# Kernel tuning notes

Measured on AMD Instinct MI355X. Metric: run time of the kernel, lower is better.

The kernel has to match this reference:

```python
import jax, jax.numpy as jnp
import numpy as np

B, T, C = 2, 4096, 512
H, DH = 8, 64            # num_heads, num_head_channels (per-head dim after reshape)
COND = 512
SCALE = (DH // H) ** -0.5  # faithful to original: (num_head_channels // num_heads)**-0.5


def setup_inputs() -> dict:
    key = jax.random.key(0)
    ks = jax.random.split(key, 6)
    x = jax.random.normal(ks[0], (B, T, C), dtype=jnp.float32)
    condition = jax.random.normal(ks[1], (B, T, COND), dtype=jnp.float32)
    W_qk = jax.random.normal(ks[2], (COND, 2 * H * DH), dtype=jnp.float32) * (COND ** -0.5)
    W_v = jax.random.normal(ks[3], (C, H * DH), dtype=jnp.float32) * (C ** -0.5)
    W_u = jax.random.normal(ks[4], (H * DH, C), dtype=jnp.float32) * ((H * DH) ** -0.5)
    b_u = jax.random.normal(ks[5], (C,), dtype=jnp.float32) * 0.01
    return {"x": x, "condition": condition, "W_qk": W_qk, "W_v": W_v, "W_u": W_u, "b_u": b_u}


def reference(x, condition, W_qk, W_v, W_u, b_u):
    b, t, _ = x.shape
    qk = condition @ W_qk                                  # [b, t, 2*H*DH]
    q, k = jnp.split(qk, 2, axis=-1)
    q = q.reshape(b, t, H, DH).transpose(0, 2, 1, 3)       # [b, H, t, DH]
    k = k.reshape(b, t, H, DH).transpose(0, 2, 1, 3)
    v = (x @ W_v).reshape(b, t, H, DH).transpose(0, 2, 1, 3)
    q = q * SCALE
    dots = jnp.einsum('bhid,bhjd->bhij', q, k)             # [b, H, t, t] (1 GB score matrix)
    attn = jax.nn.softmax(dots, axis=-1)
    out = jnp.einsum('bhij,bhjd->bhid', attn, v)           # [b, H, t, DH]
    out = out.transpose(0, 2, 1, 3).reshape(b, t, H * DH)
    return out @ W_u + b_u
```

## Files before the change

kernel.cpp:

```cpp
#include <hip/hip_runtime.h>

#define B_SZ 2
#define T_SZ 4096

typedef unsigned short u16;
typedef __attribute__((ext_vector_type(8))) short short8;
typedef __attribute__((ext_vector_type(4))) float f32x4;
typedef __attribute__((ext_vector_type(4))) unsigned short u16x4;

#define CEXP 0.51006973f

__device__ __forceinline__ u16 f2bf(float f) {
    unsigned int u;
    __builtin_memcpy(&u, &f, 4);
    u = (u + 0x7fffu + ((u >> 16) & 1u)) >> 16;
    return (u16)u;
}
__device__ __forceinline__ unsigned int rbits(float f) {
    unsigned int u;
    __builtin_memcpy(&u, &f, 4);
    return u + 0x8000u;
}
__device__ __forceinline__ f32x4 mfma16(short8 a, short8 b, f32x4 c) {
    return __builtin_amdgcn_mfma_f32_16x16x32_bf16(a, b, c, 0, 0, 0);
}

__global__ void k_prep(const float* __restrict__ Wqk, const float* __restrict__ Wv,
                       const float* __restrict__ Wu, u16* __restrict__ Wqk_t,
                       u16* __restrict__ Wv_t, u16* __restrict__ Wu_t) {
    int blk = blockIdx.x;
    if (blk < 2048) {
        int idx = blk * 256 + threadIdx.x;
        Wqk_t[(size_t)(idx & 1023) * 512 + (idx >> 10)] = f2bf(Wqk[idx]);
    } else if (blk < 3072) {
        int idx = (blk - 2048) * 256 + threadIdx.x;
        Wv_t[(size_t)(idx & 511) * 512 + (idx >> 9)] = f2bf(Wv[idx]);
    } else {
        int idx = (blk - 3072) * 256 + threadIdx.x;
        Wu_t[(size_t)(idx & 511) * 512 + (idx >> 9)] = f2bf(Wu[idx]);
    }
}

template <typename OutT, int MODE, bool AF32, bool BF32, int TM, int TN>
__global__ __launch_bounds__(256) void k_gemm4(const void* __restrict__ Ap, const void* __restrict__ Bp,
                                               const float* __restrict__ bias, OutT* __restrict__ C,
                                               OutT* __restrict__ C2) {
    const int K = 512;
    constexpr int MI = TM / 32, NJ = TN / 32;
    constexpr int NAF = TM / 32, NAB = TM / 64;
    constexpr int NBF = TN / 32, NBB = TN / 64;
    int m0 = blockIdx.x * TM, n0 = blockIdx.y * TN;
    int tid = threadIdx.x;
    int wave = tid >> 6, lane = tid & 63, l16 = lane & 15, q = lane >> 4;
    int mo = (wave & 1) * (TM / 2), no = (wave >> 1) * (TN / 2);

    __shared__ __align__(16) u16 As[TM * 72];
    __shared__ __align__(16) u16 Bs[TN * 72];

    f32x4 acc[MI][NJ];
#pragma unroll
    for (int i = 0; i < MI; ++i)
#pragma unroll
        for (int j = 0; j < NJ; ++j) acc[i][j] = (f32x4){0.f, 0.f, 0.f, 0.f};

    const float* Af = (const float*)Ap; const u16* Ab = (const u16*)Ap;
    const float* Bf = (const float*)Bp; const u16* Bb = (const u16*)Bp;

    const float* apf[NAF > 0 ? NAF : 1]; const u16* apb[NAB > 0 ? NAB : 1];
    const float* bpf[NBF > 0 ? NBF : 1]; const u16* bpb[NBB > 0 ? NBB : 1];
    float4 raf[NAF > 0 ? NAF : 1], rbf[NBF > 0 ? NBF : 1];
    short8 rab[NAB > 0 ? NAB : 1], rbb[NBB > 0 ? NBB : 1];

    if constexpr (AF32) {
#pragma unroll
        for (int jj = 0; jj < NAF; ++jj) {
            int id = tid + 256 * jj;
            apf[jj] = Af + (size_t)(m0 + (id >> 3)) * K + (id & 7) * 4;
            raf[jj] = *(const float4*)(apf[jj]);
        }
    } else {
#pragma unroll
        for (int jj = 0; jj < NAB; ++jj) {
            int id = tid + 256 * jj;
            apb[jj] = Ab + (size_t)(m0 + (id >> 2)) * K + (id & 3) * 8;
            rab[jj] = *(const short8*)(apb[jj]);
        }
    }
    if constexpr (BF32) {
#pragma unroll
        for (int jj = 0; jj < NBF; ++jj) {
            int id = tid + 256 * jj;
            bpf[jj] = Bf + (size_t)(n0 + (id >> 3)) * K + (id & 7) * 4;
            rbf[jj] = *(const float4*)(bpf[jj]);
        }
    } else {
#pragma unroll
        for (int jj = 0; jj < NBB; ++jj) {
            int id = tid + 256 * jj;
            bpb[jj] = Bb + (size_t)(n0 + (id >> 2)) * K + (id & 3) * 8;
            rbb[jj] = *(const short8*)(bpb[jj]);
        }
    }

#pragma unroll 1
    for (int k0 = 0; k0 < K; k0 += 32) {
        __syncthreads();
        if constexpr (AF32) {
#pragma unroll
            for (int jj = 0; jj < NAF; ++jj) {
                int id = tid + 256 * jj;
                u16x4 w = { f2bf(raf[jj].x), f2bf(raf[jj].y), f2bf(raf[jj].z), f2bf(raf[jj].w) };
                *(u16x4*)(&As[(id >> 3) * 72 + (id & 7) * 4]) = w;
            }
        } else {
#pragma unroll
            for (int jj = 0; jj < NAB; ++jj) {
                int id = tid + 256 * jj;
                *(short8*)(&As[(id >> 2) * 72 + (id & 3) * 8]) = rab[jj];
            }
        }
        if constexpr (BF32) {
#pragma unroll
            for (int jj = 0; jj < NBF; ++jj) {
                int id = tid + 256 * jj;
                u16x4 w = { f2bf(rbf[jj].x), f2bf(rbf[jj].y), f2bf(rbf[jj].z), f2bf(rbf[jj].w) };
                *(u16x4*)(&Bs[(id >> 3) * 72 + (id & 7) * 4]) = w;
            }
        } else {
#pragma unroll
            for (int jj = 0; jj < NBB; ++jj) {
                int id = tid + 256 * jj;
                *(short8*)(&Bs[(id >> 2) * 72 + (id & 3) * 8]) = rbb[jj];
            }
        }
        __syncthreads();

        int kadv = (k0 + 32 < K) ? 32 : 0;
        if constexpr (AF32) {
#pragma unroll
            for (int jj = 0; jj < NAF; ++jj) { apf[jj] += kadv; raf[jj] = *(const float4*)(apf[jj]); }
        } else {
#pragma unroll
            for (int jj = 0; jj < NAB; ++jj) { apb[jj] += kadv; rab[jj] = *(const short8*)(apb[jj]); }
        }
        if constexpr (BF32) {
#pragma unroll
            for (int jj = 0; jj < NBF; ++jj) { bpf[jj] += kadv; rbf[jj] = *(const float4*)(bpf[jj]); }
        } else {
#pragma unroll
            for (int jj = 0; jj < NBB; ++jj) { bpb[jj] += kadv; rbb[jj] = *(const short8*)(bpb[jj]); }
        }
        __builtin_amdgcn_sched_barrier(0);

        short8 af[MI], bf[NJ];
#pragma unroll
        for (int i = 0; i < MI; ++i) af[i] = *(const short8*)(&As[(mo + i * 16 + l16) * 72 + q * 8]);
#pragma unroll
        for (int j = 0; j < NJ; ++j) bf[j] = *(const short8*)(&Bs[(no + j * 16 + l16) * 72 + q * 8]);
#pragma unroll
        for (int i = 0; i < MI; ++i)
#pragma unroll
            for (int j = 0; j < NJ; ++j) acc[i][j] = mfma16(af[i], bf[j], acc[i][j]);
    }

#pragma unroll
    for (int i = 0; i < MI; ++i) {
        int mb = m0 + mo + i * 16 + q * 4;
#pragma unroll
        for (int j = 0; j < NJ; ++j) {
            int nc = n0 + no + j * 16 + l16;
            if constexpr (MODE == 0) {
                float4 bb = *(const float4*)(bias + mb);
                float4 w = { acc[i][j][0] + bb.x, acc[i][j][1] + bb.y,
                             acc[i][j][2] + bb.z, acc[i][j][3] + bb.w };
                *(float4*)(&C[(size_t)nc * 512 + mb]) = w;
            } else if constexpr (MODE == 1) {
                int b = nc >> 12, t = nc & 4095;
                int h = (mb & 511) >> 6, d = mb & 63;
                size_t addr = ((size_t)((b * 8 + h) * 4096 + t)) * 64 + d;
                if (mb < 512) {
                    u16x4 w = { f2bf(acc[i][j][0] * CEXP), f2bf(acc[i][j][1] * CEXP),
                                f2bf(acc[i][j][2] * CEXP), f2bf(acc[i][j][3] * CEXP) };
                    *(u16x4*)(&C[addr]) = w;
                } else {
                    u16x4 w = { f2bf(acc[i][j][0]), f2bf(acc[i][j][1]),
                                f2bf(acc[i][j][2]), f2bf(acc[i][j][3]) };
                    *(u16x4*)(&C2[addr]) = w;
                }
            } else {
                int b = mb >> 12, t = mb & 4095;
                int kt = t >> 6, k64 = t & 63;
                int h = nc >> 6, d = nc & 63;
                size_t addr = ((((size_t)(b * 8 + h) * 64 + kt) * 64 + d) << 6) + k64;
                u16x4 w = { f2bf(acc[i][j][0]), f2bf(acc[i][j][1]),
                            f2bf(acc[i][j][2]), f2bf(acc[i][j][3]) };
                *(u16x4*)(&C[addr]) = w;
            }
        }
    }
}

__global__ __launch_bounds__(256) void k_flash(const u16* __restrict__ Qh, const u16* __restrict__ Kh,
                                               const u16* __restrict__ Vb, u16* __restrict__ o) {
    int bid = blockIdx.x;
    int h = bid & 7, qt = (bid >> 3) & 31, b = bid >> 8;
    int tid = threadIdx.x;
    int wave = tid >> 6, lane = tid & 63, l16 = lane & 15, q = lane >> 4;

    __shared__ __align__(16) u16 Kt[64 * 80];
    __shared__ __align__(16) u16 Vt[64 * 72];

    int head = b * 8 + h;
    short8 qf[2][2];
#pragma unroll
    for (int g = 0; g < 2; ++g) {
        const u16* qp = Qh + ((size_t)head * 4096 + qt * 128 + g * 64 + wave * 16 + l16) * 64 + q * 8;
        qf[g][0] = *(const short8*)(qp);
        qf[g][1] = *(const short8*)(qp + 32);
    }

    const u16* kb = Kh + (size_t)head * 4096 * 64;
    const u16* vb = Vb + (size_t)head * 4096 * 64;

    int r0 = tid >> 3, g0 = tid & 7;
    u16* kw0 = &Kt[r0 * 80 + g0 * 8];
    u16* kw1 = &Kt[(r0 + 32) * 80 + g0 * 8];
    u16* vw0 = &Vt[r0 * 72 + g0 * 8];
    u16* vw1 = &Vt[(r0 + 32) * 72 + g0 * 8];

    f32x4 oacc[2][4];
#pragma unroll
    for (int g = 0; g < 2; ++g)
#pragma unroll
        for (int c = 0; c < 4; ++c) oacc[g][c] = (f32x4){0.f, 0.f, 0.f, 0.f};
    f32x4 lacc[2];
    lacc[0] = (f32x4){0.f, 0.f, 0.f, 0.f};
    lacc[1] = (f32x4){0.f, 0.f, 0.f, 0.f};
    const short8 ones = { 0x3F80, 0x3F80, 0x3F80, 0x3F80, 0x3F80, 0x3F80, 0x3F80, 0x3F80 };
    int pi0 = (l16 >> 2) * 8 + (l16 & 3);

    int start = qt * 2;
    size_t off0 = (size_t)((start) & 63) * 4096;
    short8 rk0 = *(const short8*)(kb + off0 + tid * 8);
    short8 rk1 = *(const short8*)(kb + off0 + tid * 8 + 2048);
    short8 rv0 = *(const short8*)(vb + off0 + tid * 8);
    short8 rv1 = *(const short8*)(vb + off0 + tid * 8 + 2048);

#pragma unroll 1
    for (int it = 0; it < 64; ++it) {
        __syncthreads();
        *(short8*)kw0 = rk0;
        *(short8*)kw1 = rk1;
        *(short8*)vw0 = rv0;
        *(short8*)vw1 = rv1;
        __syncthreads();

        size_t offn = (size_t)((start + it + 1) & 63) * 4096;
        rk0 = *(const short8*)(kb + offn + tid * 8);
        rk1 = *(const short8*)(kb + offn + tid * 8 + 2048);
        rv0 = *(const short8*)(vb + offn + tid * 8);
        rv1 = *(const short8*)(vb + offn + tid * 8 + 2048);
        __builtin_amdgcn_sched_barrier(0);

#pragma unroll
        for (int kk = 0; kk < 2; ++kk) {
            const u16* ka = &Kt[(kk * 32 + pi0) * 80 + q * 8];
            short8 A00 = *(const short8*)(ka);
            short8 A01 = *(const short8*)(ka + 32);
            short8 A10 = *(const short8*)(ka + 4 * 80);
            short8 A11 = *(const short8*)(ka + 4 * 80 + 32);
            short8 vfc[4];
#pragma unroll
            for (int c = 0; c < 4; ++c)
                vfc[c] = *(const short8*)(&Vt[(c * 16 + l16) * 72 + kk * 32 + q * 8]);

#pragma unroll
            for (int g = 0; g < 2; ++g) {
                f32x4 s0 = (f32x4){0.f, 0.f, 0.f, 0.f};
                f32x4 s1 = (f32x4){0.f, 0.f, 0.f, 0.f};
                s0 = mfma16(A00, qf[g][0], s0); s0 = mfma16(A01, qf[g][1], s0);
                s1 = mfma16(A10, qf[g][0], s1); s1 = mfma16(A11, qf[g][1], s1);

                uint4 pd;
                pd.x = __builtin_amdgcn_perm(rbits(__builtin_amdgcn_exp2f(s0[1])),
                                             rbits(__builtin_amdgcn_exp2f(s0[0])), 0x07060302u);
                pd.y = __builtin_amdgcn_perm(rbits(__builtin_amdgcn_exp2f(s0[3])),
                                             rbits(__builtin_amdgcn_exp2f(s0[2])), 0x07060302u);
                pd.z = __builtin_amdgcn_perm(rbits(__builtin_amdgcn_exp2f(s1[1])),
                                             rbits(__builtin_amdgcn_exp2f(s1[0])), 0x07060302u);
                pd.w = __builtin_amdgcn_perm(rbits(__builtin_amdgcn_exp2f(s1[3])),
                                             rbits(__builtin_amdgcn_exp2f(s1[2])), 0x07060302u);
                short8 pf;
                __builtin_memcpy(&pf, &pd, 16);

                lacc[g] = mfma16(ones, pf, lacc[g]);
#pragma unroll
                for (int c = 0; c < 4; ++c)
                    oacc[g][c] = mfma16(vfc[c], pf, oacc[g][c]);
            }
        }
    }

#pragma unroll
    for (int g = 0; g < 2; ++g) {
        float inv = 1.f / lacc[g][0];
        u16* ob = o + (size_t)(b * T_SZ + qt * 128 + g * 64 + wave * 16 + l16) * 512 + h * 64 + q * 4;
#pragma unroll
        for (int c = 0; c < 4; ++c) {
            u16x4 w = { f2bf(oacc[g][c][0] * inv), f2bf(oacc[g][c][1] * inv),
                        f2bf(oacc[g][c][2] * inv), f2bf(oacc[g][c][3] * inv) };
            *(u16x4*)(ob + c * 16) = w;
        }
    }
}

extern "C" void kernel_launch(void* const* d_in, const int* in_sizes, int n_in,
                              void* d_out, int out_size, void* d_ws, size_t ws_size,
                              hipStream_t stream) {
    const float* x    = (const float*)d_in[0];
    const float* cond = (const float*)d_in[1];
    const float* Wqk  = (const float*)d_in[2];
    const float* Wv   = (const float*)d_in[3];
    const float* Wu   = (const float*)d_in[4];
    const float* bu   = (const float*)d_in[5];
    float* out = (float*)d_out;

    const size_t MT = (size_t)B_SZ * T_SZ;
    u16* qh_ws = (u16*)d_ws;
    u16* kh_ws = qh_ws + MT * 512;
    u16* vb_ws = kh_ws + MT * 512;
    u16* at_ws = vb_ws + MT * 512;
    u16* Wqk_t = at_ws + MT * 512;
    u16* Wv_t  = Wqk_t + (size_t)1024 * 512;
    u16* Wu_t  = Wv_t + (size_t)512 * 512;

    k_prep<<<4096, 256, 0, stream>>>(Wqk, Wv, Wu, Wqk_t, Wv_t, Wu_t);

    k_gemm4<u16, 1, false, true, 256, 64><<<dim3(4, 128), 256, 0, stream>>>(Wqk_t, cond, nullptr, qh_ws, kh_ws);
    k_gemm4<u16, 2, true, false, 64, 128><<<dim3(128, 4), 256, 0, stream>>>(x, Wv_t, nullptr, vb_ws, nullptr);
    k_flash<<<512, 256, 0, stream>>>(qh_ws, kh_ws, vb_ws, at_ws);
    k_gemm4<float, 0, false, false, 128, 64><<<dim3(4, 128), 256, 0, stream>>>(Wu_t, at_ws, bu, out, nullptr);
}
```

Baseline: 235.2 us.

## Split flash KV range across two wave groups, merge QKV GEMMs, tile weight prep

```diff
diff --git a/kernel.cpp b/kernel.cpp
--- a/kernel.cpp
+++ b/kernel.cpp
@@ -28,34 +28,43 @@
 __global__ void k_prep(const float* __restrict__ Wqk, const float* __restrict__ Wv,
                        const float* __restrict__ Wu, u16* __restrict__ Wqk_t,
                        u16* __restrict__ Wv_t, u16* __restrict__ Wu_t) {
-    int blk = blockIdx.x;
-    if (blk < 2048) {
-        int idx = blk * 256 + threadIdx.x;
-        Wqk_t[(size_t)(idx & 1023) * 512 + (idx >> 10)] = f2bf(Wqk[idx]);
-    } else if (blk < 3072) {
-        int idx = (blk - 2048) * 256 + threadIdx.x;
-        Wv_t[(size_t)(idx & 511) * 512 + (idx >> 9)] = f2bf(Wv[idx]);
-    } else {
-        int idx = (blk - 3072) * 256 + threadIdx.x;
-        Wu_t[(size_t)(idx & 511) * 512 + (idx >> 9)] = f2bf(Wu[idx]);
+    int blk = blockIdx.x, tid = threadIdx.x;
+    __shared__ u16 T[64][72];
+    const float* src; u16* dst; int N, ti;
+    if (blk < 128)      { src = Wqk; dst = Wqk_t; N = 1024; ti = blk; }
+    else if (blk < 192) { src = Wv;  dst = Wv_t;  N = 512;  ti = blk - 128; }
+    else                { src = Wu;  dst = Wu_t;  N = 512;  ti = blk - 192; }
+    int nt = N >> 6;
+    int bi = ti / nt, bj = ti - bi * nt;
+    int kb = bi * 64, nb = bj * 64;
+    int r = tid >> 2, c4 = (tid & 3) * 16;
+#pragma unroll
+    for (int jj = 0; jj < 4; ++jj) {
+        float4 v = *(const float4*)(src + (size_t)(kb + r) * N + nb + c4 + jj * 4);
+        u16x4 w = { f2bf(v.x), f2bf(v.y), f2bf(v.z), f2bf(v.w) };
+        *(u16x4*)(&T[r][c4 + jj * 4]) = w;
+    }
+    __syncthreads();
+#pragma unroll
+    for (int jj = 0; jj < 4; ++jj) {
+        int c = c4 + jj * 4;
+        u16x4 w = { T[c][r], T[c + 1][r], T[c + 2][r], T[c + 3][r] };
+        *(u16x4*)(dst + (size_t)(nb + r) * 512 + kb + c) = w;
     }
 }
 
 template <typename OutT, int MODE, bool AF32, bool BF32, int TM, int TN>
-__global__ __launch_bounds__(256) void k_gemm4(const void* __restrict__ Ap, const void* __restrict__ Bp,
-                                               const float* __restrict__ bias, OutT* __restrict__ C,
-                                               OutT* __restrict__ C2) {
+__device__ __forceinline__ void gemm_body(int m0, int n0,
+                                          const void* __restrict__ Ap, const void* __restrict__ Bp,
+                                          const float* __restrict__ bias, OutT* __restrict__ C,
+                                          OutT* __restrict__ C2, u16* As, u16* Bs) {
     const int K = 512;
     constexpr int MI = TM / 32, NJ = TN / 32;
     constexpr int NAF = TM / 32, NAB = TM / 64;
     constexpr int NBF = TN / 32, NBB = TN / 64;
-    int m0 = blockIdx.x * TM, n0 = blockIdx.y * TN;
     int tid = threadIdx.x;
     int wave = tid >> 6, lane = tid & 63, l16 = lane & 15, q = lane >> 4;
     int mo = (wave & 1) * (TM / 2), no = (wave >> 1) * (TN / 2);
-
-    __shared__ __align__(16) u16 As[TM * 72];
-    __shared__ __align__(16) u16 Bs[TN * 72];
 
     f32x4 acc[MI][NJ];
 #pragma unroll
@@ -200,21 +209,51 @@
     }
 }
 
-__global__ __launch_bounds__(256) void k_flash(const u16* __restrict__ Qh, const u16* __restrict__ Kh,
+__global__ __launch_bounds__(256) void k_qkv(const u16* __restrict__ Wqk_t, const float* __restrict__ cond,
+                                             const float* __restrict__ x, const u16* __restrict__ Wv_t,
+                                             u16* __restrict__ Qh, u16* __restrict__ Kh,
+                                             u16* __restrict__ Vb) {
+    __shared__ __align__(16) u16 smem[(128 + 64) * 72];
+    u16* As = smem;
+    u16* Bs = smem + 128 * 72;
+    int bid = blockIdx.x;
+    if (bid < 1024) {
+        int bx = bid >> 7, by = bid & 127;
+        gemm_body<u16, 1, false, true, 128, 64>(bx * 128, by * 64, Wqk_t, cond, nullptr, Qh, Kh, As, Bs);
+    } else {
+        int bid2 = bid - 1024;
+        int by = bid2 >> 6, bx = bid2 & 63;
+        gemm_body<u16, 2, true, false, 128, 64>(bx * 128, by * 64, x, Wv_t, nullptr, Vb, nullptr, As, Bs);
+    }
+}
+
+__global__ __launch_bounds__(256) void k_out(const u16* __restrict__ Wu_t, const u16* __restrict__ at,
+                                             const float* __restrict__ bu, float* __restrict__ out) {
+    __shared__ __align__(16) u16 smem[(64 + 64) * 72];
+    int bid = blockIdx.x;
+    int bx = bid >> 7, by = bid & 127;
+    gemm_body<float, 0, false, false, 64, 64>(bx * 64, by * 64, Wu_t, at, bu, out, nullptr,
+                                              smem, smem + 64 * 72);
+}
+
+__global__ __launch_bounds__(512) void k_flash(const u16* __restrict__ Qh, const u16* __restrict__ Kh,
                                                const u16* __restrict__ Vb, u16* __restrict__ o) {
     int bid = blockIdx.x;
     int h = bid & 7, qt = (bid >> 3) & 31, b = bid >> 8;
     int tid = threadIdx.x;
     int wave = tid >> 6, lane = tid & 63, l16 = lane & 15, q = lane >> 4;
-
-    __shared__ __align__(16) u16 Kt[64 * 80];
-    __shared__ __align__(16) u16 Vt[64 * 72];
+    int ks = wave >> 2, w4 = wave & 3;
+    int t256 = tid & 255;
+
+    __shared__ __align__(16) u16 smem[2 * (64 * 80 + 64 * 72)];
+    u16* Kt = smem + ks * (64 * 80 + 64 * 72);
+    u16* Vt = Kt + 64 * 80;
 
     int head = b * 8 + h;
     short8 qf[2][2];
 #pragma unroll
     for (int g = 0; g < 2; ++g) {
-        const u16* qp = Qh + ((size_t)head * 4096 + qt * 128 + g * 64 + wave * 16 + l16) * 64 + q * 8;
+        const u16* qp = Qh + ((size_t)head * 4096 + qt * 128 + g * 64 + w4 * 16 + l16) * 64 + q * 8;
         qf[g][0] = *(const short8*)(qp);
         qf[g][1] = *(const short8*)(qp + 32);
     }
@@ -222,7 +261,7 @@
     const u16* kb = Kh + (size_t)head * 4096 * 64;
     const u16* vb = Vb + (size_t)head * 4096 * 64;
 
-    int r0 = tid >> 3, g0 = tid & 7;
+    int r0 = t256 >> 3, g0 = t256 & 7;
     u16* kw0 = &Kt[r0 * 80 + g0 * 8];
     u16* kw1 = &Kt[(r0 + 32) * 80 + g0 * 8];
     u16* vw0 = &Vt[r0 * 72 + g0 * 8];
@@ -239,15 +278,14 @@
     const short8 ones = { 0x3F80, 0x3F80, 0x3F80, 0x3F80, 0x3F80, 0x3F80, 0x3F80, 0x3F80 };
     int pi0 = (l16 >> 2) * 8 + (l16 & 3);
 
-    int start = qt * 2;
-    size_t off0 = (size_t)((start) & 63) * 4096;
-    short8 rk0 = *(const short8*)(kb + off0 + tid * 8);
-    short8 rk1 = *(const short8*)(kb + off0 + tid * 8 + 2048);
-    short8 rv0 = *(const short8*)(vb + off0 + tid * 8);
-    short8 rv1 = *(const short8*)(vb + off0 + tid * 8 + 2048);
+    size_t off0 = (size_t)(ks * 32 + (qt & 31)) * 4096;
+    short8 rk0 = *(const short8*)(kb + off0 + t256 * 8);
+    short8 rk1 = *(const short8*)(kb + off0 + t256 * 8 + 2048);
+    short8 rv0 = *(const short8*)(vb + off0 + t256 * 8);
+    short8 rv1 = *(const short8*)(vb + off0 + t256 * 8 + 2048);
 
 #pragma unroll 1
-    for (int it = 0; it < 64; ++it) {
+    for (int it = 0; it < 32; ++it) {
         __syncthreads();
         *(short8*)kw0 = rk0;
         *(short8*)kw1 = rk1;
@@ -255,11 +293,11 @@
         *(short8*)vw1 = rv1;
         __syncthreads();
 
-        size_t offn = (size_t)((start + it + 1) & 63) * 4096;
-        rk0 = *(const short8*)(kb + offn + tid * 8);
-        rk1 = *(const short8*)(kb + offn + tid * 8 + 2048);
-        rv0 = *(const short8*)(vb + offn + tid * 8);
-        rv1 = *(const short8*)(vb + offn + tid * 8 + 2048);
+        size_t offn = (size_t)(ks * 32 + ((qt + it + 1) & 31)) * 4096;
+        rk0 = *(const short8*)(kb + offn + t256 * 8);
+        rk1 = *(const short8*)(kb + offn + t256 * 8 + 2048);
+        rv0 = *(const short8*)(vb + offn + t256 * 8);
+        rv1 = *(const short8*)(vb + offn + t256 * 8 + 2048);
         __builtin_amdgcn_sched_barrier(0);
 
 #pragma unroll
@@ -301,15 +339,36 @@
         }
     }
 
-#pragma unroll
-    for (int g = 0; g < 2; ++g) {
-        float inv = 1.f / lacc[g][0];
-        u16* ob = o + (size_t)(b * T_SZ + qt * 128 + g * 64 + wave * 16 + l16) * 512 + h * 64 + q * 4;
-#pragma unroll
-        for (int c = 0; c < 4; ++c) {
-            u16x4 w = { f2bf(oacc[g][c][0] * inv), f2bf(oacc[g][c][1] * inv),
-                        f2bf(oacc[g][c][2] * inv), f2bf(oacc[g][c][3] * inv) };
-            *(u16x4*)(ob + c * 16) = w;
+    __syncthreads();
+    float* red = (float*)smem;
+    if (ks == 1) {
+        float* rp = red + ((w4 * 64 + lane) * 37);
+#pragma unroll
+        for (int g = 0; g < 2; ++g)
+#pragma unroll
+            for (int c = 0; c < 4; ++c)
+#pragma unroll
+                for (int r = 0; r < 4; ++r) rp[g * 16 + c * 4 + r] = oacc[g][c][r];
+        rp[32] = lacc[0][0];
+        rp[33] = lacc[1][0];
+    }
+    __syncthreads();
+    if (ks == 0) {
+        const float* rp = red + ((w4 * 64 + lane) * 37);
+#pragma unroll
+        for (int g = 0; g < 2; ++g) {
+#pragma unroll
+            for (int c = 0; c < 4; ++c)
+#pragma unroll
+                for (int r = 0; r < 4; ++r) oacc[g][c][r] += rp[g * 16 + c * 4 + r];
+            float inv = 1.f / (lacc[g][0] + rp[32 + g]);
+            u16* ob = o + (size_t)(b * T_SZ + qt * 128 + g * 64 + w4 * 16 + l16) * 512 + h * 64 + q * 4;
+#pragma unroll
+            for (int c = 0; c < 4; ++c) {
+                u16x4 w = { f2bf(oacc[g][c][0] * inv), f2bf(oacc[g][c][1] * inv),
+                            f2bf(oacc[g][c][2] * inv), f2bf(oacc[g][c][3] * inv) };
+                *(u16x4*)(ob + c * 16) = w;
+            }
         }
     }
 }
@@ -334,10 +393,8 @@
     u16* Wv_t  = Wqk_t + (size_t)1024 * 512;
     u16* Wu_t  = Wv_t + (size_t)512 * 512;
 
-    k_prep<<<4096, 256, 0, stream>>>(Wqk, Wv, Wu, Wqk_t, Wv_t, Wu_t);
-
-    k_gemm4<u16, 1, false, true, 256, 64><<<dim3(4, 128), 256, 0, stream>>>(Wqk_t, cond, nullptr, qh_ws, kh_ws);
-    k_gemm4<u16, 2, true, false, 64, 128><<<dim3(128, 4), 256, 0, stream>>>(x, Wv_t, nullptr, vb_ws, nullptr);
-    k_flash<<<512, 256, 0, stream>>>(qh_ws, kh_ws, vb_ws, at_ws);
-    k_gemm4<float, 0, false, false, 128, 64><<<dim3(4, 128), 256, 0, stream>>>(Wu_t, at_ws, bu, out, nullptr);
-}
+    k_prep<<<256, 256, 0, stream>>>(Wqk, Wv, Wu, Wqk_t, Wv_t, Wu_t);
+    k_qkv<<<1536, 256, 0, stream>>>(Wqk_t, cond, x, Wv_t, qh_ws, kh_ws, vb_ws);
+    k_flash<<<512, 512, 0, stream>>>(qh_ws, kh_ws, vb_ws, at_ws);
+    k_out<<<1024, 256, 0, stream>>>(Wu_t, at_ws, bu, out);
+}
```

Result: faster. 212.8 us (-9.5%).
